# Optimization experiments

Measured on AMD Instinct MI355X. Metric: run time of the kernel, lower is better.

Reference implementation:

```python
import jax, jax.numpy as jnp
import numpy as np

B, N, E = 32, 128, 8192
IMG, LOC, H = 2048, 5, 128


def setup_inputs() -> dict:
    key = jax.random.key(0)
    ks = jax.random.split(key, 10)
    img_feat = jax.random.normal(ks[0], (B, N, IMG), dtype=jnp.float32)
    img_loc = jax.random.uniform(ks[1], (B, N, LOC), dtype=jnp.float32)
    edge_src = jax.random.randint(ks[2], (E,), 0, N, dtype=jnp.int32)
    edge_dst = jax.random.randint(ks[3], (E,), 0, N, dtype=jnp.int32)
    # learned parameters (nn.Linear: y = x @ W + b)
    W_img = jax.random.normal(ks[4], (IMG, H), dtype=jnp.float32) / np.sqrt(IMG)
    b_img = jnp.zeros((H,), dtype=jnp.float32)
    W_loc = jax.random.normal(ks[5], (LOC, H), dtype=jnp.float32) / np.sqrt(LOC)
    b_loc = jnp.zeros((H,), dtype=jnp.float32)
    W_rel = jax.random.normal(ks[6], (2 * H, H), dtype=jnp.float32) / np.sqrt(2 * H)
    b_rel = jnp.zeros((H,), dtype=jnp.float32)
    return {
        "img_feat": img_feat, "img_loc": img_loc,
        "edge_src": edge_src, "edge_dst": edge_dst,
        "W_img": W_img, "b_img": b_img,
        "W_loc": W_loc, "b_loc": b_loc,
        "W_rel": W_rel, "b_rel": b_rel,
    }


def reference(img_feat, img_loc, edge_src, edge_dst,
              W_img, b_img, W_loc, b_loc, W_rel, b_rel):
    # img_fc / img_loc_fc projections
    img = jnp.einsum('bni,ih->bnh', img_feat, W_img) + b_img      # [B,N,H]
    loc = jnp.einsum('bnl,lh->bnh', img_loc, W_loc) + b_loc       # [B,N,H]
    node_feat = img + loc                                          # [B,N,H]
    # per-edge gather + concat + linear (batched over all edges at once;
    # split W_rel to avoid materializing the concat)
    src_f = jnp.take(img, edge_src, axis=1)                        # [B,E,H]
    dst_f = jnp.take(img, edge_dst, axis=1)                        # [B,E,H]
    edge_feat = (jnp.einsum('beh,hk->bek', src_f, W_rel[:H]) +
                 jnp.einsum('beh,hk->bek', dst_f, W_rel[H:]) + b_rel)  # [B,E,H]
    return node_feat, edge_feat
```

## Files before the change

### kernel.cpp

```cpp
#include <hip/hip_runtime.h>
#include <hip/hip_bf16.h>
#include <stdint.h>

#define B_   32
#define N_   128
#define E_   8192
#define IMG_ 2048
#define H_   128

typedef __attribute__((ext_vector_type(8))) short bf16x8;
typedef __attribute__((ext_vector_type(4))) float f32x4;

__device__ inline uint16_t f2bf(float x) {
    uint32_t u = __float_as_uint(x);
    uint32_t r = (u + 0x7FFFu + ((u >> 16) & 1u)) >> 16;
    return (uint16_t)r;
}
__device__ inline float bf2f(short x) {
    return __uint_as_float(((uint32_t)(uint16_t)x) << 16);
}

__global__ __launch_bounds__(256) void prep_kernel(
    const float* __restrict__ W_img, const float* __restrict__ W_rel,
    uint16_t* __restrict__ Wt_img, uint16_t* __restrict__ Wt_rel) {
    int bid = blockIdx.x, tid = threadIdx.x;
    if (bid < 32) {
        __shared__ float t[64][129];
        int k0 = bid * 64;
        const float* src = W_img + (size_t)k0 * H_;
        #pragma unroll
        for (int it = 0; it < 32; it++) {
            int idx = it * 256 + tid;
            t[idx >> 7][idx & 127] = src[idx];
        }
        __syncthreads();
        int c = tid >> 1, kh = (tid & 1) * 32;
        uint16_t* dst = Wt_img + (size_t)c * IMG_ + k0 + kh;
        #pragma unroll
        for (int j = 0; j < 32; j++) dst[j] = f2bf(t[kh + j][c]);
    } else {
        int t2 = (bid - 32) * 256 + tid;
        int c = t2 >> 8, k = t2 & 255;
        Wt_rel[t2] = f2bf(W_rel[k * H_ + c]);
    }
}

__global__ __launch_bounds__(1024) void node_proj_kernel(
    const float* __restrict__ img_feat,
    const uint16_t* __restrict__ Wt_img,
    const uint16_t* __restrict__ Wt_rel,
    const float* __restrict__ img_loc,
    const float* __restrict__ b_img,
    const float* __restrict__ W_loc,
    const float* __restrict__ b_loc,
    const float* __restrict__ b_rel,
    float* __restrict__ out_node,
    uint16_t* __restrict__ proj) {
    __shared__ __align__(16) char lds_raw[131072];
    float (*red)[16][128] = (float (*)[16][128])lds_raw;
    uint16_t (*imgb)[136] = (uint16_t (*)[136])lds_raw;

    int strip = blockIdx.x;
    int tid = threadIdx.x;
    int w  = tid >> 6;
    int l  = tid & 63;
    int lr = l & 15;
    int kq = l >> 4;

    const char* gA = (const char*)(img_feat + (size_t)strip * 16 * IMG_);
    #pragma unroll
    for (int r = 0; r < 8; r++) {
        int L = r * 16384 + tid * 16;
        int row = L >> 13;
        int koff = L & 8191;
        int gsrc = row * 8192 + (koff ^ ((row & 7) << 4));
        __builtin_amdgcn_global_load_lds(
            (const __attribute__((address_space(1))) void*)(gA + gsrc),
            (__attribute__((address_space(3))) void*)(lds_raw + L), 16, 0, 0);
    }

    int kbase = w * 128 + kq * 8;
    bf16x8 bcur[8];
    #pragma unroll
    for (int n = 0; n < 8; n++)
        bcur[n] = *(const bf16x8*)(Wt_img + (size_t)(n * 16 + lr) * IMG_ + kbase);

    __syncthreads();

    f32x4 acc[8];
    #pragma unroll
    for (int n = 0; n < 8; n++) acc[n] = (f32x4){0.f, 0.f, 0.f, 0.f};
    int sw = (lr & 7) << 4;
    #pragma unroll
    for (int ks = 0; ks < 4; ks++) {
        int koffb = w * 512 + ks * 128 + kq * 32;
        float4 a0 = *(const float4*)(lds_raw + (size_t)lr * 8192 + (koffb ^ sw));
        float4 a1 = *(const float4*)(lds_raw + (size_t)lr * 8192 + ((koffb + 16) ^ sw));
        bf16x8 bn[8];
        if (ks < 3) {
            int kn = kbase + (ks + 1) * 32;
            #pragma unroll
            for (int n = 0; n < 8; n++)
                bn[n] = *(const bf16x8*)(Wt_img + (size_t)(n * 16 + lr) * IMG_ + kn);
        }
        bf16x8 af;
        af[0] = (short)f2bf(a0.x); af[1] = (short)f2bf(a0.y);
        af[2] = (short)f2bf(a0.z); af[3] = (short)f2bf(a0.w);
        af[4] = (short)f2bf(a1.x); af[5] = (short)f2bf(a1.y);
        af[6] = (short)f2bf(a1.z); af[7] = (short)f2bf(a1.w);
        #pragma unroll
        for (int n = 0; n < 8; n++)
            acc[n] = __builtin_amdgcn_mfma_f32_16x16x32_bf16(af, bcur[n], acc[n], 0, 0, 0);
        if (ks < 3) {
            #pragma unroll
            for (int n = 0; n < 8; n++) bcur[n] = bn[n];
        }
    }
    __syncthreads();

    #pragma unroll
    for (int n = 0; n < 8; n++)
        #pragma unroll
        for (int r = 0; r < 4; r++)
            red[w][kq * 4 + r][n * 16 + lr] = acc[n][r];
    __syncthreads();

    int row0 = tid >> 7, col = tid & 127;
    int row1 = row0 + 8;
    float s0 = 0.f, s1 = 0.f;
    #pragma unroll
    for (int ww = 0; ww < 16; ww++) {
        s0 += red[ww][row0][col];
        s1 += red[ww][row1][col];
    }
    __syncthreads();

    {
        float bi = b_img[col];
        float bl = b_loc[col];
        float wl[5];
        #pragma unroll
        for (int j = 0; j < 5; j++) wl[j] = W_loc[j * H_ + col];
        float img0 = s0 + bi, img1 = s1 + bi;
        int g0 = strip * 16 + row0, g1 = strip * 16 + row1;
        const float* lc0 = img_loc + g0 * 5;
        const float* lc1 = img_loc + g1 * 5;
        float loc0 = bl, loc1 = bl;
        #pragma unroll
        for (int j = 0; j < 5; j++) { loc0 += lc0[j] * wl[j]; loc1 += lc1[j] * wl[j]; }
        out_node[(size_t)g0 * H_ + col] = img0 + loc0;
        out_node[(size_t)g1 * H_ + col] = img1 + loc1;
        imgb[row0][col] = f2bf(img0);
        imgb[row1][col] = f2bf(img1);
    }
    __syncthreads();

    int kl = kq * 8;
    int cp = w * 16 + lr;
    const uint16_t* bbase = (cp < 128)
        ? (Wt_rel + (size_t)cp * 256)
        : (Wt_rel + (size_t)(cp - 128) * 256 + 128);
    f32x4 pacc = (f32x4){0.f, 0.f, 0.f, 0.f};
    #pragma unroll
    for (int ks = 0; ks < 4; ks++) {
        int k = ks * 32 + kl;
        bf16x8 af = *(const bf16x8*)(&imgb[lr][k]);
        bf16x8 bf = *(const bf16x8*)(bbase + k);
        pacc = __builtin_amdgcn_mfma_f32_16x16x32_bf16(af, bf, pacc, 0, 0, 0);
    }
    float brel = (cp < 128) ? b_rel[cp] : 0.f;
    #pragma unroll
    for (int r = 0; r < 4; r++) {
        int grow = strip * 16 + kq * 4 + r;
        proj[(size_t)grow * 256 + cp] = f2bf(pacc[r] + brel);
    }
}

__global__ __launch_bounds__(256) void edge_kernel(
    const uint16_t* __restrict__ proj,
    const int* __restrict__ edge_src,
    const int* __restrict__ edge_dst,
    float* __restrict__ out_edge) {
    int t = blockIdx.x * 256 + threadIdx.x;
    int b0 = t >> 17;
    int r  = t & 131071;
    int e  = r >> 4;
    int c  = (r & 15) * 8;
    int s  = edge_src[e];
    int d  = edge_dst[e];
    const uint16_t* ps = proj + ((size_t)(b0 * N_ + s) * 256 + c);
    const uint16_t* pd = proj + ((size_t)(b0 * N_ + d) * 256 + 128 + c);
    float* op = out_edge + ((size_t)(b0 * E_ + e) * H_ + c);
    const size_t PSTR = (size_t)4 * N_ * 256;
    const size_t OSTR = (size_t)4 * E_ * H_;

    #pragma unroll
    for (int h = 0; h < 2; h++) {
        bf16x8 av[4], bv[4];
        #pragma unroll
        for (int i = 0; i < 4; i++) {
            size_t it = (size_t)(h * 4 + i);
            av[i] = *(const bf16x8*)(ps + it * PSTR);
            bv[i] = *(const bf16x8*)(pd + it * PSTR);
        }
        #pragma unroll
        for (int i = 0; i < 4; i++) {
            size_t it = (size_t)(h * 4 + i);
            float4 o0, o1;
            o0.x = bf2f(av[i][0]) + bf2f(bv[i][0]);
            o0.y = bf2f(av[i][1]) + bf2f(bv[i][1]);
            o0.z = bf2f(av[i][2]) + bf2f(bv[i][2]);
            o0.w = bf2f(av[i][3]) + bf2f(bv[i][3]);
            o1.x = bf2f(av[i][4]) + bf2f(bv[i][4]);
            o1.y = bf2f(av[i][5]) + bf2f(bv[i][5]);
            o1.z = bf2f(av[i][6]) + bf2f(bv[i][6]);
            o1.w = bf2f(av[i][7]) + bf2f(bv[i][7]);
            float* dst = op + it * OSTR;
            *(float4*)dst = o0;
            *(float4*)(dst + 4) = o1;
        }
    }
}

extern "C" void kernel_launch(void* const* d_in, const int* in_sizes, int n_in,
                              void* d_out, int out_size, void* d_ws, size_t ws_size,
                              hipStream_t stream) {
    const float* img_feat = (const float*)d_in[0];
    const float* img_loc  = (const float*)d_in[1];
    const int*   edge_src = (const int*)d_in[2];
    const int*   edge_dst = (const int*)d_in[3];
    const float* W_img    = (const float*)d_in[4];
    const float* b_img    = (const float*)d_in[5];
    const float* W_loc    = (const float*)d_in[6];
    const float* b_loc    = (const float*)d_in[7];
    const float* W_rel    = (const float*)d_in[8];
    const float* b_rel    = (const float*)d_in[9];

    float* out_node = (float*)d_out;
    float* out_edge = out_node + (size_t)B_ * N_ * H_;

    char* ws = (char*)d_ws;
    uint16_t* Wt_img = (uint16_t*)ws;
    uint16_t* Wt_rel = (uint16_t*)(ws + 524288);
    uint16_t* proj   = (uint16_t*)(ws + 524288 + 65536);

    prep_kernel<<<dim3(160), dim3(256), 0, stream>>>(W_img, W_rel, Wt_img, Wt_rel);

    node_proj_kernel<<<dim3(256), dim3(1024), 0, stream>>>(
        img_feat, Wt_img, Wt_rel, img_loc, b_img, W_loc, b_loc, b_rel,
        out_node, proj);

    edge_kernel<<<dim3(2048), dim3(256), 0, stream>>>(
        proj, edge_src, edge_dst, out_edge);
}
```

Baseline: 58.56 us.

## Split node projection into 8-row strips across 512 blocks of 512 threads

The node projection kernel now handles 8 rows per block instead of 16 and launches 512 blocks of 512 threads, using 64KB of LDS instead of 128KB. Each wave covers a quarter of K and half of the output columns, which cuts the cross-wave reduction from 16 partials to 4. The aim is to double the block count so more CUs are busy and LDS pressure drops. The cost is that the 16-row MFMA tiles are half wasted (rows duplicated via lr&7) and the weights are re-read by twice as many blocks.

After: 73.06 us. +24.8%, slower.

```diff
diff --git a/kernel.cpp b/kernel.cpp
--- a/kernel.cpp
+++ b/kernel.cpp
@@ -45,7 +45,7 @@
     }
 }
 
-__global__ __launch_bounds__(1024) void node_proj_kernel(
+__global__ __launch_bounds__(512) void node_proj_kernel(
     const float* __restrict__ img_feat,
     const uint16_t* __restrict__ Wt_img,
     const uint16_t* __restrict__ Wt_rel,
@@ -56,52 +56,57 @@
     const float* __restrict__ b_rel,
     float* __restrict__ out_node,
     uint16_t* __restrict__ proj) {
-    __shared__ __align__(16) char lds_raw[131072];
-    float (*red)[16][128] = (float (*)[16][128])lds_raw;
-    uint16_t (*imgb)[136] = (uint16_t (*)[136])lds_raw;
+    __shared__ __align__(16) char lds_raw[65536];
+    __shared__ __align__(16) uint16_t imgb[8][136];
 
     int strip = blockIdx.x;
     int tid = threadIdx.x;
     int w  = tid >> 6;
+    int kw = w & 3;
+    int ch = w >> 2;
     int l  = tid & 63;
     int lr = l & 15;
     int kq = l >> 4;
-
-    const char* gA = (const char*)(img_feat + (size_t)strip * 16 * IMG_);
+    int row8 = lr & 7;
+
+    float (*red)[8][128] = (float (*)[8][128])lds_raw;
+
+    const char* gA = (const char*)(img_feat + (size_t)strip * 8 * IMG_);
     #pragma unroll
     for (int r = 0; r < 8; r++) {
-        int L = r * 16384 + tid * 16;
+        int L = r * 8192 + tid * 16;
         int row = L >> 13;
         int koff = L & 8191;
-        int gsrc = row * 8192 + (koff ^ ((row & 7) << 4));
+        int gsrc = row * 8192 + (koff ^ (row << 4));
         __builtin_amdgcn_global_load_lds(
             (const __attribute__((address_space(1))) void*)(gA + gsrc),
             (__attribute__((address_space(3))) void*)(lds_raw + L), 16, 0, 0);
     }
 
-    int kbase = w * 128 + kq * 8;
-    bf16x8 bcur[8];
-    #pragma unroll
-    for (int n = 0; n < 8; n++)
-        bcur[n] = *(const bf16x8*)(Wt_img + (size_t)(n * 16 + lr) * IMG_ + kbase);
-
-    __syncthreads();
-
-    f32x4 acc[8];
-    #pragma unroll
-    for (int n = 0; n < 8; n++) acc[n] = (f32x4){0.f, 0.f, 0.f, 0.f};
-    int sw = (lr & 7) << 4;
-    #pragma unroll
-    for (int ks = 0; ks < 4; ks++) {
-        int koffb = w * 512 + ks * 128 + kq * 32;
-        float4 a0 = *(const float4*)(lds_raw + (size_t)lr * 8192 + (koffb ^ sw));
-        float4 a1 = *(const float4*)(lds_raw + (size_t)lr * 8192 + ((koffb + 16) ^ sw));
-        bf16x8 bn[8];
-        if (ks < 3) {
+    int kbase = kw * 512 + kq * 8;
+    const uint16_t* wbase = Wt_img + (size_t)(ch * 64) * IMG_;
+    bf16x8 bcur[4];
+    #pragma unroll
+    for (int n = 0; n < 4; n++)
+        bcur[n] = *(const bf16x8*)(wbase + (size_t)(n * 16 + lr) * IMG_ + kbase);
+
+    __syncthreads();
+
+    f32x4 acc[4];
+    #pragma unroll
+    for (int n = 0; n < 4; n++) acc[n] = (f32x4){0.f, 0.f, 0.f, 0.f};
+    int sw = row8 << 4;
+    #pragma unroll
+    for (int ks = 0; ks < 16; ks++) {
+        int koffb = kw * 2048 + ks * 128 + kq * 32;
+        float4 a0 = *(const float4*)(lds_raw + row8 * 8192 + (koffb ^ sw));
+        float4 a1 = *(const float4*)(lds_raw + row8 * 8192 + ((koffb + 16) ^ sw));
+        bf16x8 bn[4];
+        if (ks < 15) {
             int kn = kbase + (ks + 1) * 32;
             #pragma unroll
-            for (int n = 0; n < 8; n++)
-                bn[n] = *(const bf16x8*)(Wt_img + (size_t)(n * 16 + lr) * IMG_ + kn);
+            for (int n = 0; n < 4; n++)
+                bn[n] = *(const bf16x8*)(wbase + (size_t)(n * 16 + lr) * IMG_ + kn);
         }
         bf16x8 af;
         af[0] = (short)f2bf(a0.x); af[1] = (short)f2bf(a0.y);
@@ -109,32 +114,33 @@
         af[4] = (short)f2bf(a1.x); af[5] = (short)f2bf(a1.y);
         af[6] = (short)f2bf(a1.z); af[7] = (short)f2bf(a1.w);
         #pragma unroll
-        for (int n = 0; n < 8; n++)
+        for (int n = 0; n < 4; n++)
             acc[n] = __builtin_amdgcn_mfma_f32_16x16x32_bf16(af, bcur[n], acc[n], 0, 0, 0);
-        if (ks < 3) {
-            #pragma unroll
-            for (int n = 0; n < 8; n++) bcur[n] = bn[n];
-        }
-    }
-    __syncthreads();
-
-    #pragma unroll
-    for (int n = 0; n < 8; n++)
-        #pragma unroll
-        for (int r = 0; r < 4; r++)
-            red[w][kq * 4 + r][n * 16 + lr] = acc[n][r];
-    __syncthreads();
-
-    int row0 = tid >> 7, col = tid & 127;
-    int row1 = row0 + 8;
+        if (ks < 15) {
+            #pragma unroll
+            for (int n = 0; n < 4; n++) bcur[n] = bn[n];
+        }
+    }
+    __syncthreads();
+
+    if (kq < 2) {
+        #pragma unroll
+        for (int n = 0; n < 4; n++)
+            #pragma unroll
+            for (int r = 0; r < 4; r++)
+                red[kw][kq * 4 + r][ch * 64 + n * 16 + lr] = acc[n][r];
+    }
+    __syncthreads();
+
+    int col = tid & 127;
+    int row0 = tid >> 7;
+    int row1 = row0 + 4;
     float s0 = 0.f, s1 = 0.f;
     #pragma unroll
-    for (int ww = 0; ww < 16; ww++) {
-        s0 += red[ww][row0][col];
-        s1 += red[ww][row1][col];
-    }
-    __syncthreads();
-
+    for (int p = 0; p < 4; p++) {
+        s0 += red[p][row0][col];
+        s1 += red[p][row1][col];
+    }
     {
         float bi = b_img[col];
         float bl = b_loc[col];
@@ -142,7 +148,7 @@
         #pragma unroll
         for (int j = 0; j < 5; j++) wl[j] = W_loc[j * H_ + col];
         float img0 = s0 + bi, img1 = s1 + bi;
-        int g0 = strip * 16 + row0, g1 = strip * 16 + row1;
+        int g0 = strip * 8 + row0, g1 = strip * 8 + row1;
         const float* lc0 = img_loc + g0 * 5;
         const float* lc1 = img_loc + g1 * 5;
         float loc0 = bl, loc1 = bl;
@@ -155,24 +161,37 @@
     }
     __syncthreads();
 
-    int kl = kq * 8;
-    int cp = w * 16 + lr;
-    const uint16_t* bbase = (cp < 128)
-        ? (Wt_rel + (size_t)cp * 256)
-        : (Wt_rel + (size_t)(cp - 128) * 256 + 128);
-    f32x4 pacc = (f32x4){0.f, 0.f, 0.f, 0.f};
-    #pragma unroll
-    for (int ks = 0; ks < 4; ks++) {
-        int k = ks * 32 + kl;
-        bf16x8 af = *(const bf16x8*)(&imgb[lr][k]);
-        bf16x8 bf = *(const bf16x8*)(bbase + k);
-        pacc = __builtin_amdgcn_mfma_f32_16x16x32_bf16(af, bf, pacc, 0, 0, 0);
-    }
-    float brel = (cp < 128) ? b_rel[cp] : 0.f;
-    #pragma unroll
-    for (int r = 0; r < 4; r++) {
-        int grow = strip * 16 + kq * 4 + r;
-        proj[(size_t)grow * 256 + cp] = f2bf(pacc[r] + brel);
+    {
+        int kl = kq * 8;
+        int cp0 = w * 32 + lr;
+        int cp1 = cp0 + 16;
+        const uint16_t* bb0 = (cp0 < 128)
+            ? (Wt_rel + (size_t)cp0 * 256)
+            : (Wt_rel + (size_t)(cp0 - 128) * 256 + 128);
+        const uint16_t* bb1 = (cp1 < 128)
+            ? (Wt_rel + (size_t)cp1 * 256)
+            : (Wt_rel + (size_t)(cp1 - 128) * 256 + 128);
+        f32x4 p0 = (f32x4){0.f, 0.f, 0.f, 0.f};
+        f32x4 p1 = p0;
+        #pragma unroll
+        for (int ks = 0; ks < 4; ks++) {
+            int k = ks * 32 + kl;
+            bf16x8 af = *(const bf16x8*)(&imgb[row8][k]);
+            bf16x8 bf0 = *(const bf16x8*)(bb0 + k);
+            bf16x8 bf1 = *(const bf16x8*)(bb1 + k);
+            p0 = __builtin_amdgcn_mfma_f32_16x16x32_bf16(af, bf0, p0, 0, 0, 0);
+            p1 = __builtin_amdgcn_mfma_f32_16x16x32_bf16(af, bf1, p1, 0, 0, 0);
+        }
+        float br0 = (cp0 < 128) ? b_rel[cp0] : 0.f;
+        float br1 = (cp1 < 128) ? b_rel[cp1] : 0.f;
+        if (kq < 2) {
+            #pragma unroll
+            for (int r = 0; r < 4; r++) {
+                int grow = strip * 8 + kq * 4 + r;
+                proj[(size_t)grow * 256 + cp0] = f2bf(p0[r] + br0);
+                proj[(size_t)grow * 256 + cp1] = f2bf(p1[r] + br1);
+            }
+        }
     }
 }
 
@@ -246,7 +265,7 @@
 
     prep_kernel<<<dim3(160), dim3(256), 0, stream>>>(W_img, W_rel, Wt_img, Wt_rel);
 
-    node_proj_kernel<<<dim3(256), dim3(1024), 0, stream>>>(
+    node_proj_kernel<<<dim3(512), dim3(512), 0, stream>>>(
         img_feat, Wt_img, Wt_rel, img_loc, b_img, W_loc, b_loc, b_rel,
         out_node, proj);
 
```
